# Kernel tuning notes

Measured on AMD Instinct MI355X. Metric: run time of the kernel, lower is better.

## Reference

```python
import jax, jax.numpy as jnp
import numpy as np
import math

B, N, DIM = 16, 1024, 384
DEPTH, HEADS, DH = 6, 6, 64
INNER = HEADS * DH          # 384
MLP = 1536
LN_EPS = 1e-5


def setup_inputs() -> dict:
    key = jax.random.key(0)
    ks = jax.random.split(key, 7)
    s = 0.02
    x = jax.random.normal(ks[0], (B, N, DIM), dtype=jnp.float32)
    ln1_g = jnp.ones((DEPTH, DIM), jnp.float32)
    ln1_b = jnp.zeros((DEPTH, DIM), jnp.float32)
    qkv_w = jax.random.normal(ks[1], (DEPTH, DIM, 3 * INNER), jnp.float32) * s
    temp = jnp.full((DEPTH,), math.log(DH ** -0.5), jnp.float32)
    out_w = jax.random.normal(ks[2], (DEPTH, INNER, DIM), jnp.float32) * s
    out_b = jnp.zeros((DEPTH, DIM), jnp.float32)
    ln2_g = jnp.ones((DEPTH, DIM), jnp.float32)
    ln2_b = jnp.zeros((DEPTH, DIM), jnp.float32)
    ff_w1 = jax.random.normal(ks[3], (DEPTH, DIM, MLP), jnp.float32) * s
    ff_b1 = jnp.zeros((DEPTH, MLP), jnp.float32)
    ff_w2 = jax.random.normal(ks[4], (DEPTH, MLP, DIM), jnp.float32) * s
    ff_b2 = jnp.zeros((DEPTH, DIM), jnp.float32)
    return dict(x=x, ln1_g=ln1_g, ln1_b=ln1_b, qkv_w=qkv_w, temp=temp,
                out_w=out_w, out_b=out_b, ln2_g=ln2_g, ln2_b=ln2_b,
                ff_w1=ff_w1, ff_b1=ff_b1, ff_w2=ff_w2, ff_b2=ff_b2)


def _ln(x, g, b):
    m = jnp.mean(x, axis=-1, keepdims=True)
    v = jnp.var(x, axis=-1, keepdims=True)
    return (x - m) * jax.lax.rsqrt(v + LN_EPS) * g + b


def reference(x, ln1_g, ln1_b, qkv_w, temp, out_w, out_b,
              ln2_g, ln2_b, ff_w1, ff_b1, ff_w2, ff_b2):
    neg = -jnp.finfo(x.dtype).max
    eye = jnp.eye(N, dtype=bool)

    def step(x, p):
        g1, b1, wqkv, t, wo, bo, g2, b2, w1, bb1, w2, bb2 = p
        # --- PreNorm + LSA attention ---
        h = _ln(x, g1, b1)
        qkv = h @ wqkv                              # [B, N, 3*INNER]
        q, k, v = jnp.split(qkv, 3, axis=-1)
        split_heads = lambda a: a.reshape(B, N, HEADS, DH).transpose(0, 2, 1, 3)
        q, k, v = split_heads(q), split_heads(k), split_heads(v)
        dots = jnp.einsum('bhnd,bhmd->bhnm', q, k) * jnp.exp(t)
        dots = jnp.where(eye, neg, dots)            # mask diagonal (LSA)
        attn = jax.nn.softmax(dots, axis=-1)
        o = jnp.einsum('bhnm,bhmd->bhnd', attn, v)
        o = o.transpose(0, 2, 1, 3).reshape(B, N, INNER)
        x = x + o @ wo + bo
        # --- PreNorm + FeedForward (exact GELU) ---
        h2 = _ln(x, g2, b2)
        ff = jax.nn.gelu(h2 @ w1 + bb1, approximate=False) @ w2 + bb2
        x = x + ff
        return x, None

    params = (ln1_g, ln1_b, qkv_w, temp, out_w, out_b,
              ln2_g, ln2_b, ff_w1, ff_b1, ff_w2, ff_b2)
    x, _ = jax.lax.scan(step, x, params)
    return x
```

## Files before the change

### kernel.cpp

```cpp
#include <hip/hip_runtime.h>
#include <hip/hip_bf16.h>
#include <math.h>

#define B_     16
#define NTOK   1024
#define DIM_   384
#define DEPTH_ 6
#define HEADS_ 6
#define DH_    64
#define MLP_   1536
#define MTOT   (B_ * NTOK)
#define NBH    (B_ * HEADS_)
#define QKV_PLANE ((size_t)NBH * NTOK * DH_)

typedef unsigned short u16;
typedef unsigned int u32;
typedef short short8 __attribute__((ext_vector_type(8)));
typedef float f32x4 __attribute__((ext_vector_type(4)));

static __device__ __forceinline__ u16 f2b(float f) {
    __hip_bfloat16 h = __float2bfloat16(f);
    return *reinterpret_cast<u16*>(&h);
}

#define GLOAD_LDS16(gp, lp)                                                     \
    __builtin_amdgcn_global_load_lds(                                           \
        (const __attribute__((address_space(1))) void*)(gp),                    \
        (__attribute__((address_space(3))) void*)(lp), 16, 0, 0)

#define WAIT_VM(N)                                                              \
    do { asm volatile("s_waitcnt vmcnt(" #N ")" ::: "memory");                  \
         __builtin_amdgcn_sched_barrier(0); } while (0)
#define WAIT_LGKM0()                                                            \
    do { asm volatile("s_waitcnt lgkmcnt(0)" ::: "memory");                     \
         __builtin_amdgcn_sched_barrier(0); } while (0)

__launch_bounds__(256)
__global__ void transpose_w_kernel(const float* __restrict__ W, u16* __restrict__ WT,
                                   int K, int N) {
    const int layer = blockIdx.z;
    W  += (size_t)layer * K * N;
    WT += (size_t)layer * K * N;
    __shared__ u16 tile[64 * 72];
    const int t = threadIdx.x;
    const int k0 = blockIdx.x * 64, n0 = blockIdx.y * 64;
    const int row = t >> 2, cs = (t & 3) * 16;
    const float4* src = reinterpret_cast<const float4*>(W + (size_t)(k0 + row) * N + n0 + cs);
#pragma unroll
    for (int i = 0; i < 4; i++) {
        float4 f = src[i];
        tile[row * 72 + cs + i * 4 + 0] = f2b(f.x);
        tile[row * 72 + cs + i * 4 + 1] = f2b(f.y);
        tile[row * 72 + cs + i * 4 + 2] = f2b(f.z);
        tile[row * 72 + cs + i * 4 + 3] = f2b(f.w);
    }
    __syncthreads();
    const int nrow = row, ks = cs;
    u16 vals[16] __attribute__((aligned(16)));
#pragma unroll
    for (int e = 0; e < 16; e++) vals[e] = tile[(ks + e) * 72 + nrow];
    u16* dst = WT + (size_t)(n0 + nrow) * K + k0 + ks;
    *reinterpret_cast<short8*>(dst)     = *reinterpret_cast<short8*>(&vals[0]);
    *reinterpret_cast<short8*>(dst + 8) = *reinterpret_cast<short8*>(&vals[8]);
}

__launch_bounds__(256)
__global__ void ln_kernel(const float* __restrict__ x, const float* __restrict__ g,
                          const float* __restrict__ b, u16* __restrict__ h) {
    const int tok  = blockIdx.x * 4 + (threadIdx.x >> 6);
    const int lane = threadIdx.x & 63;
    const float* xr = x + (size_t)tok * DIM_;
    float v[6];
    float s = 0.f;
#pragma unroll
    for (int i = 0; i < 6; i++) { v[i] = xr[lane + i * 64]; s += v[i]; }
#pragma unroll
    for (int m = 1; m < 64; m <<= 1) s += __shfl_xor(s, m);
    const float mean = s * (1.f / 384.f);
    float qs = 0.f;
#pragma unroll
    for (int i = 0; i < 6; i++) { float d = v[i] - mean; qs += d * d; }
#pragma unroll
    for (int m = 1; m < 64; m <<= 1) qs += __shfl_xor(qs, m);
    const float inv = rsqrtf(qs * (1.f / 384.f) + 1e-5f);
    u16* hr = h + (size_t)tok * DIM_;
#pragma unroll
    for (int i = 0; i < 6; i++) {
        const int c = lane + i * 64;
        hr[c] = f2b((v[i] - mean) * inv * g[c] + b[c]);
    }
}

enum { EPI_QKV = 0, EPI_RES = 1, EPI_GELU = 2 };

template <int EPI>
__launch_bounds__(256)
__global__ void gemm_kernel(const u16* __restrict__ A, const u16* __restrict__ BT, int K,
                            int ntn,
                            const float* __restrict__ bias, const float* __restrict__ resid,
                            float* __restrict__ outf, u16* __restrict__ outb, int ldc,
                            u16* __restrict__ qkv_base) {
    __shared__ u16 As[3][4096];
    __shared__ u16 Bs[3][4096];
    const int t = threadIdx.x;
    const int lane = t & 63, w = t >> 6;
    const int wm = w >> 1, wn = w & 1;

    const int cpx = (int)gridDim.x >> 3;
    const int swz = ((int)blockIdx.x & 7) * cpx + ((int)blockIdx.x >> 3);
    const int m0 = (swz / ntn) * 128, n0 = (swz % ntn) * 128;

    f32x4 acc[4][4] = {};

    const int c0p = w * 1024, c1p = w * 1024 + 512;
    const int seg = (lane & 3) * 8;
    const u16* agp0 = A  + (size_t)(m0 + (w * 2 + 0) * 16 + (lane >> 2)) * K + seg;
    const u16* agp1 = A  + (size_t)(m0 + (w * 2 + 1) * 16 + (lane >> 2)) * K + seg;
    const u16* bgp0 = BT + (size_t)(n0 + (w * 2 + 0) * 16 + (lane >> 2)) * K + seg;
    const u16* bgp1 = BT + (size_t)(n0 + (w * 2 + 1) * 16 + (lane >> 2)) * K + seg;

    const int T = K >> 5;
    GLOAD_LDS16(agp0,      &As[0][c0p]);
    GLOAD_LDS16(agp1,      &As[0][c1p]);
    GLOAD_LDS16(bgp0,      &Bs[0][c0p]);
    GLOAD_LDS16(bgp1,      &Bs[0][c1p]);
    GLOAD_LDS16(agp0 + 32, &As[1][c0p]);
    GLOAD_LDS16(agp1 + 32, &As[1][c1p]);
    GLOAD_LDS16(bgp0 + 32, &Bs[1][c0p]);
    GLOAD_LDS16(bgp1 + 32, &Bs[1][c1p]);

    int b0 = 0, b1 = 1, b2 = 2;
    for (int tt = 0; tt < T; ++tt) {
        if (tt + 2 < T) {
            const int kk = (tt + 2) << 5;
            GLOAD_LDS16(agp0 + kk, &As[b2][c0p]);
            GLOAD_LDS16(agp1 + kk, &As[b2][c1p]);
            GLOAD_LDS16(bgp0 + kk, &Bs[b2][c0p]);
            GLOAD_LDS16(bgp1 + kk, &Bs[b2][c1p]);
            WAIT_VM(8);
        } else if (tt + 1 < T) {
            WAIT_VM(4);
        } else {
            WAIT_VM(0);
        }
        __builtin_amdgcn_s_barrier();
        short8 af[4], bf[4];
#pragma unroll
        for (int i = 0; i < 4; i++)
            af[i] = *reinterpret_cast<const short8*>(
                &As[b0][(wm * 64 + i * 16 + (lane & 15)) * 32 + (lane >> 4) * 8]);
#pragma unroll
        for (int j = 0; j < 4; j++)
            bf[j] = *reinterpret_cast<const short8*>(
                &Bs[b0][(wn * 64 + j * 16 + (lane & 15)) * 32 + (lane >> 4) * 8]);
#pragma unroll
        for (int i = 0; i < 4; i++)
#pragma unroll
            for (int j = 0; j < 4; j++)
                acc[i][j] = __builtin_amdgcn_mfma_f32_16x16x32_bf16(af[i], bf[j], acc[i][j], 0, 0, 0);
        WAIT_LGKM0();
        __builtin_amdgcn_s_barrier();
        const int tmp = b0; b0 = b1; b1 = b2; b2 = tmp;
    }

    const int rbase = (lane >> 4) * 4;
    const int cb = lane & 15;
#pragma unroll
    for (int i = 0; i < 4; i++) {
#pragma unroll
        for (int j = 0; j < 4; j++) {
            if constexpr (EPI == EPI_QKV) {
                const int c = n0 + wn * 64 + j * 16 + cb;
                const int which = c / 384;
                const int cc = c - which * 384;
                const int head = cc >> 6, dh = cc & 63;
                const int nb = m0 + wm * 64 + i * 16 + rbase;
                const int b = nb >> 10, nt = nb & 1023;
                const size_t bh = (size_t)(b * HEADS_ + head);
                if (which == 2) {
                    u16 pk[4] __attribute__((aligned(8)));
#pragma unroll
                    for (int r = 0; r < 4; r++) pk[r] = f2b(acc[i][j][r]);
                    const int nsw = (nt & ~63) | ((((nt >> 3) & 7) ^ (dh & 7)) << 3) | (nt & 7);
                    *reinterpret_cast<uint2*>(
                        &qkv_base[2 * QKV_PLANE + bh * 65536 + (size_t)dh * 1024 + nsw]) =
                        *reinterpret_cast<uint2*>(pk);
                } else if (which == 1) {
#pragma unroll
                    for (int r = 0; r < 4; r++) {
                        const int n = nt + r;
                        const int dsw = (((dh >> 3) ^ (n & 7)) << 3) | (dh & 7);
                        qkv_base[QKV_PLANE + bh * 65536 + (size_t)n * 64 + dsw] =
                            f2b(acc[i][j][r]);
                    }
                } else {
#pragma unroll
                    for (int r = 0; r < 4; r++)
                        qkv_base[bh * 65536 + (size_t)(nt + r) * 64 + dh] = f2b(acc[i][j][r]);
                }
            } else {
#pragma unroll
                for (int r = 0; r < 4; r++) {
                    const int m = m0 + wm * 64 + i * 16 + rbase + r;
                    const int c = n0 + wn * 64 + j * 16 + cb;
                    const float val = acc[i][j][r];
                    if constexpr (EPI == EPI_RES) {
                        outf[(size_t)m * ldc + c] = resid[(size_t)m * ldc + c] + bias[c] + val;
                    } else {
                        const float xg = val + bias[c];
                        const float y = 0.7978845608f * (xg + 0.044715f * xg * xg * xg);
                        const float e = __expf(2.0f * fabsf(y));
                        float th = 1.0f - 2.0f / (e + 1.0f);
                        th = copysignf(th, y);
                        outb[(size_t)m * ldc + c] = f2b(0.5f * xg * (1.0f + th));
                    }
                }
            }
        }
    }
}

__launch_bounds__(256)
__global__ void attn_kernel(const u16* __restrict__ q, const u16* __restrict__ k,
                            const u16* __restrict__ v, const float* __restrict__ temp,
                            u16* __restrict__ o) {
    __shared__ u16 Kt[2][4096];
    __shared__ u16 Vt[2][4096];
    __shared__ u16 Ps[4][16 * 80];
    const int t = threadIdx.x, lane = t & 63, w = t >> 6;
    const int g8 = lane >> 4, qi = lane & 15;
    const int bh = blockIdx.x, q0 = blockIdx.y * 64;
    const float scale2 = __expf(temp[0]) * 1.4426950408889634f;
    const size_t base = (size_t)bh * (NTOK * DH_);

    short8 bq[2];
#pragma unroll
    for (int s = 0; s < 2; s++)
        bq[s] = *reinterpret_cast<const short8*>(
            &q[base + (size_t)(q0 + w * 16 + qi) * 64 + s * 32 + g8 * 8]);

    float m_s = -3.0e38f, l_s = 0.f;
    f32x4 accO[4] = {};
    const int qglob = q0 + w * 16 + qi;

    const int srow = w * 8 + (lane >> 3);
    const int schunk = (lane & 7) * 8;
    const u16* kg0 = k + base + (size_t)srow * 64 + schunk;
    const u16* vg0 = v + base + (size_t)srow * 1024 + schunk;
    const int wp = w * 512;

    GLOAD_LDS16(kg0,             &Kt[0][wp]);
    GLOAD_LDS16(kg0 + 32 * 64,   &Kt[0][wp + 2048]);
    GLOAD_LDS16(vg0,             &Vt[0][wp]);
    GLOAD_LDS16(vg0 + 32 * 1024, &Vt[0][wp + 2048]);

    int cur = 0;
    for (int jt = 0; jt < 16; ++jt) {
        if (jt + 1 < 16) {
            const size_t jn = (size_t)(jt + 1) * 64;
            GLOAD_LDS16(kg0 + jn * 64,            &Kt[cur ^ 1][wp]);
            GLOAD_LDS16(kg0 + jn * 64 + 32 * 64,  &Kt[cur ^ 1][wp + 2048]);
            GLOAD_LDS16(vg0 + jn,                 &Vt[cur ^ 1][wp]);
            GLOAD_LDS16(vg0 + jn + 32 * 1024,     &Vt[cur ^ 1][wp + 2048]);
            WAIT_VM(4);
        } else {
            WAIT_VM(0);
        }
        __builtin_amdgcn_s_barrier();

        f32x4 sf[4] = {};
#pragma unroll
        for (int c = 0; c < 4; c++) {
            const int krow = c * 16 + qi;
#pragma unroll
            for (int s = 0; s < 2; s++) {
                short8 af = *reinterpret_cast<const short8*>(
                    &Kt[cur][krow * 64 + (((s * 4 + g8) ^ (krow & 7)) << 3)]);
                sf[c] = __builtin_amdgcn_mfma_f32_16x16x32_bf16(af, bq[s], sf[c], 0, 0, 0);
            }
        }

        float p[4][4];
        float vmax = -3.0e38f;
        if (jt * 64 == q0) {
#pragma unroll
            for (int c = 0; c < 4; c++)
#pragma unroll
                for (int r = 0; r < 4; r++) {
                    float sv = sf[c][r] * scale2;
                    if (jt * 64 + c * 16 + g8 * 4 + r == qglob) sv = -3.0e37f;
                    p[c][r] = sv;
                    vmax = fmaxf(vmax, sv);
                }
        } else {
#pragma unroll
            for (int c = 0; c < 4; c++)
#pragma unroll
                for (int r = 0; r < 4; r++) {
                    const float sv = sf[c][r] * scale2;
                    p[c][r] = sv;
                    vmax = fmaxf(vmax, sv);
                }
        }
        vmax = fmaxf(vmax, __shfl_xor(vmax, 16));
        vmax = fmaxf(vmax, __shfl_xor(vmax, 32));

        if (!__all(vmax - m_s <= 11.0f)) {
            const float mnew = fmaxf(m_s, vmax);
            const float alpha = exp2f(m_s - mnew);
            m_s = mnew;
            l_s *= alpha;
#pragma unroll
            for (int r = 0; r < 4; r++) {
                const float a_r = __shfl(alpha, g8 * 4 + r, 64);
#pragma unroll
                for (int g = 0; g < 4; g++) accO[g][r] *= a_r;
            }
        }

        float tsum = 0.f;
#pragma unroll
        for (int c = 0; c < 4; c++)
#pragma unroll
            for (int r = 0; r < 4; r++) {
                const float pe = exp2f(p[c][r] - m_s);
                p[c][r] = pe;
                tsum += pe;
            }
        tsum += __shfl_xor(tsum, 16);
        tsum += __shfl_xor(tsum, 32);
        l_s += tsum;

#pragma unroll
        for (int c = 0; c < 4; c++) {
            u32 lo = (u32)f2b(p[c][0]) | ((u32)f2b(p[c][1]) << 16);
            u32 hi = (u32)f2b(p[c][2]) | ((u32)f2b(p[c][3]) << 16);
            uint2 pr; pr.x = lo; pr.y = hi;
            *reinterpret_cast<uint2*>(&Ps[w][qi * 80 + c * 16 + g8 * 4]) = pr;
        }

#pragma unroll
        for (int s = 0; s < 2; s++) {
            short8 ap = *reinterpret_cast<const short8*>(&Ps[w][qi * 80 + s * 32 + g8 * 8]);
#pragma unroll
            for (int g = 0; g < 4; g++) {
                const int vrow = g * 16 + qi;
                short8 bv = *reinterpret_cast<const short8*>(
                    &Vt[cur][vrow * 64 + (((s * 4 + g8) ^ (vrow & 7)) << 3)]);
                accO[g] = __builtin_amdgcn_mfma_f32_16x16x32_bf16(ap, bv, accO[g], 0, 0, 0);
            }
        }
        WAIT_LGKM0();
        __builtin_amdgcn_s_barrier();
        cur ^= 1;
    }

    const int bidx = bh / HEADS_, head = bh % HEADS_;
#pragma unroll
    for (int r = 0; r < 4; r++) {
        const float li = __shfl(l_s, g8 * 4 + r, 64);
        const float linv = 1.f / li;
        const int n = q0 + w * 16 + g8 * 4 + r;
#pragma unroll
        for (int g = 0; g < 4; g++) {
            const int dh = g * 16 + qi;
            o[((size_t)(bidx * NTOK + n)) * DIM_ + head * DH_ + dh] = f2b(accO[g][r] * linv);
        }
    }
}

extern "C" void kernel_launch(void* const* d_in, const int* in_sizes, int n_in,
                              void* d_out, int out_size, void* d_ws, size_t ws_size,
                              hipStream_t stream) {
    const float* x_in  = (const float*)d_in[0];
    const float* ln1_g = (const float*)d_in[1];
    const float* ln1_b = (const float*)d_in[2];
    const float* qkv_w = (const float*)d_in[3];
    const float* temp  = (const float*)d_in[4];
    const float* out_w = (const float*)d_in[5];
    const float* out_b = (const float*)d_in[6];
    const float* ln2_g = (const float*)d_in[7];
    const float* ln2_b = (const float*)d_in[8];
    const float* ff_w1 = (const float*)d_in[9];
    const float* ff_b1 = (const float*)d_in[10];
    const float* ff_w2 = (const float*)d_in[11];
    const float* ff_b2 = (const float*)d_in[12];

    char* ws = (char*)d_ws;
    size_t off = 0;
    auto alloc = [&](size_t bytes) -> void* {
        void* p = ws + off;
        off += (bytes + 255) & ~(size_t)255;
        return p;
    };
    u16* wt_qkv = (u16*)alloc((size_t)DEPTH_ * 1152 * 384 * 2);
    u16* wt_out = (u16*)alloc((size_t)DEPTH_ * 384 * 384 * 2);
    u16* wt_ff1 = (u16*)alloc((size_t)DEPTH_ * 1536 * 384 * 2);
    u16* wt_ff2 = (u16*)alloc((size_t)DEPTH_ * 384 * 1536 * 2);
    u16* H      = (u16*)alloc((size_t)MTOT * DIM_ * 2);
    u16* QKV    = (u16*)alloc((size_t)MTOT * MLP_ * 2);
    u16* MID    = QKV;

    float* X = (float*)d_out;

    hipMemcpyAsync(X, x_in, (size_t)MTOT * DIM_ * sizeof(float),
                   hipMemcpyDeviceToDevice, stream);

    transpose_w_kernel<<<dim3(6, 18, DEPTH_), 256, 0, stream>>>(qkv_w, wt_qkv, 384, 1152);
    transpose_w_kernel<<<dim3(6, 6, DEPTH_), 256, 0, stream>>>(out_w, wt_out, 384, 384);
    transpose_w_kernel<<<dim3(6, 24, DEPTH_), 256, 0, stream>>>(ff_w1, wt_ff1, 384, 1536);
    transpose_w_kernel<<<dim3(24, 6, DEPTH_), 256, 0, stream>>>(ff_w2, wt_ff2, 1536, 384);

    for (int layer = 0; layer < DEPTH_; layer++) {
        ln_kernel<<<4096, 256, 0, stream>>>(X, ln1_g + layer * DIM_, ln1_b + layer * DIM_, H);
        gemm_kernel<EPI_QKV><<<dim3(128 * 9), 256, 0, stream>>>(
            H, wt_qkv + (size_t)layer * 1152 * 384, 384, 9,
            nullptr, nullptr, nullptr, nullptr, 0, QKV);
        attn_kernel<<<dim3(96, 16), 256, 0, stream>>>(
            QKV, QKV + QKV_PLANE, QKV + 2 * QKV_PLANE, temp + layer, H);
        gemm_kernel<EPI_RES><<<dim3(128 * 3), 256, 0, stream>>>(
            H, wt_out + (size_t)layer * 384 * 384, 384, 3,
            out_b + layer * DIM_, X, X, nullptr, DIM_, nullptr);
        ln_kernel<<<4096, 256, 0, stream>>>(X, ln2_g + layer * DIM_, ln2_b + layer * DIM_, H);
        gemm_kernel<EPI_GELU><<<dim3(128 * 12), 256, 0, stream>>>(
            H, wt_ff1 + (size_t)layer * 1536 * 384, 384, 12,
            ff_b1 + layer * MLP_, nullptr, nullptr, MID, MLP_, nullptr);
        gemm_kernel<EPI_RES><<<dim3(128 * 3), 256, 0, stream>>>(
            MID, wt_ff2 + (size_t)layer * 384 * 1536, 1536, 3,
            ff_b2 + layer * DIM_, X, X, nullptr, DIM_, nullptr);
    }
}
```

Before: 1.407 ms.

## Shrink GEMM tile to 128x64 with double buffering for more blocks and occupancy

The GEMM output tile is narrowed from 128x128 to 128x64, and LDS buffering drops from triple to double. Launch bounds now request 5 blocks per SM. Grid sizes double so the mostly small-N GEMMs (N=384) get more blocks and better CU coverage. The cost is less operand reuse per block, more A-tile reloads, and a shallower prefetch pipeline.

```diff
diff --git a/kernel.cpp b/kernel.cpp
--- a/kernel.cpp
+++ b/kernel.cpp
@@ -94,83 +94,75 @@
 enum { EPI_QKV = 0, EPI_RES = 1, EPI_GELU = 2 };
 
 template <int EPI>
-__launch_bounds__(256)
+__launch_bounds__(256, 5)
 __global__ void gemm_kernel(const u16* __restrict__ A, const u16* __restrict__ BT, int K,
                             int ntn,
                             const float* __restrict__ bias, const float* __restrict__ resid,
                             float* __restrict__ outf, u16* __restrict__ outb, int ldc,
                             u16* __restrict__ qkv_base) {
-    __shared__ u16 As[3][4096];
-    __shared__ u16 Bs[3][4096];
+    __shared__ u16 As[2][4096];
+    __shared__ u16 Bs[2][2048];
     const int t = threadIdx.x;
     const int lane = t & 63, w = t >> 6;
+    const int qi = lane & 15, g8 = lane >> 4;
     const int wm = w >> 1, wn = w & 1;
 
     const int cpx = (int)gridDim.x >> 3;
     const int swz = ((int)blockIdx.x & 7) * cpx + ((int)blockIdx.x >> 3);
-    const int m0 = (swz / ntn) * 128, n0 = (swz % ntn) * 128;
-
-    f32x4 acc[4][4] = {};
-
-    const int c0p = w * 1024, c1p = w * 1024 + 512;
+    const int m0 = (swz / ntn) * 128, n0 = (swz % ntn) * 64;
+
+    f32x4 acc[4][2] = {};
+
     const int seg = (lane & 3) * 8;
     const u16* agp0 = A  + (size_t)(m0 + (w * 2 + 0) * 16 + (lane >> 2)) * K + seg;
     const u16* agp1 = A  + (size_t)(m0 + (w * 2 + 1) * 16 + (lane >> 2)) * K + seg;
-    const u16* bgp0 = BT + (size_t)(n0 + (w * 2 + 0) * 16 + (lane >> 2)) * K + seg;
-    const u16* bgp1 = BT + (size_t)(n0 + (w * 2 + 1) * 16 + (lane >> 2)) * K + seg;
+    const u16* bgp  = BT + (size_t)(n0 + w * 16 + (lane >> 2)) * K + seg;
+    const int a0p = (w * 2) * 512, a1p = (w * 2 + 1) * 512, bp = w * 512;
 
     const int T = K >> 5;
-    GLOAD_LDS16(agp0,      &As[0][c0p]);
-    GLOAD_LDS16(agp1,      &As[0][c1p]);
-    GLOAD_LDS16(bgp0,      &Bs[0][c0p]);
-    GLOAD_LDS16(bgp1,      &Bs[0][c1p]);
-    GLOAD_LDS16(agp0 + 32, &As[1][c0p]);
-    GLOAD_LDS16(agp1 + 32, &As[1][c1p]);
-    GLOAD_LDS16(bgp0 + 32, &Bs[1][c0p]);
-    GLOAD_LDS16(bgp1 + 32, &Bs[1][c1p]);
-
-    int b0 = 0, b1 = 1, b2 = 2;
+    GLOAD_LDS16(agp0, &As[0][a0p]);
+    GLOAD_LDS16(agp1, &As[0][a1p]);
+    GLOAD_LDS16(bgp,  &Bs[0][bp]);
+
+    int cur = 0;
     for (int tt = 0; tt < T; ++tt) {
-        if (tt + 2 < T) {
-            const int kk = (tt + 2) << 5;
-            GLOAD_LDS16(agp0 + kk, &As[b2][c0p]);
-            GLOAD_LDS16(agp1 + kk, &As[b2][c1p]);
-            GLOAD_LDS16(bgp0 + kk, &Bs[b2][c0p]);
-            GLOAD_LDS16(bgp1 + kk, &Bs[b2][c1p]);
-            WAIT_VM(8);
-        } else if (tt + 1 < T) {
-            WAIT_VM(4);
+        if (tt + 1 < T) {
+            const int kk = (tt + 1) << 5;
+            GLOAD_LDS16(agp0 + kk, &As[cur ^ 1][a0p]);
+            GLOAD_LDS16(agp1 + kk, &As[cur ^ 1][a1p]);
+            GLOAD_LDS16(bgp + kk,  &Bs[cur ^ 1][bp]);
+            WAIT_VM(3);
         } else {
             WAIT_VM(0);
         }
         __builtin_amdgcn_s_barrier();
-        short8 af[4], bf[4];
+        short8 af[4], bf[2];
 #pragma unroll
         for (int i = 0; i < 4; i++)
             af[i] = *reinterpret_cast<const short8*>(
-                &As[b0][(wm * 64 + i * 16 + (lane & 15)) * 32 + (lane >> 4) * 8]);
-#pragma unroll
-        for (int j = 0; j < 4; j++)
+                &As[cur][(wm * 64 + i * 16 + qi) * 32 + g8 * 8]);
+#pragma unroll
+        for (int j = 0; j < 2; j++)
             bf[j] = *reinterpret_cast<const short8*>(
-                &Bs[b0][(wn * 64 + j * 16 + (lane & 15)) * 32 + (lane >> 4) * 8]);
+                &Bs[cur][(wn * 32 + j * 16 + qi) * 32 + g8 * 8]);
 #pragma unroll
         for (int i = 0; i < 4; i++)
 #pragma unroll
-            for (int j = 0; j < 4; j++)
+            for (int j = 0; j < 2; j++)
                 acc[i][j] = __builtin_amdgcn_mfma_f32_16x16x32_bf16(af[i], bf[j], acc[i][j], 0, 0, 0);
         WAIT_LGKM0();
         __builtin_amdgcn_s_barrier();
-        const int tmp = b0; b0 = b1; b1 = b2; b2 = tmp;
-    }
-
-    const int rbase = (lane >> 4) * 4;
-    const int cb = lane & 15;
+        cur ^= 1;
+    }
+
+    const int rbase = g8 * 4;
+    const int cb = qi;
 #pragma unroll
     for (int i = 0; i < 4; i++) {
 #pragma unroll
-        for (int j = 0; j < 4; j++) {
+        for (int j = 0; j < 2; j++) {
             if constexpr (EPI == EPI_QKV) {
-                const int c = n0 + wn * 64 + j * 16 + cb;
+                const int c = n0 + wn * 32 + j * 16 + cb;
                 const int which = c / 384;
                 const int cc = c - which * 384;
                 const int head = cc >> 6, dh = cc & 63;
@@ -202,7 +194,7 @@
 #pragma unroll
                 for (int r = 0; r < 4; r++) {
                     const int m = m0 + wm * 64 + i * 16 + rbase + r;
-                    const int c = n0 + wn * 64 + j * 16 + cb;
+                    const int c = n0 + wn * 32 + j * 16 + cb;
                     const float val = acc[i][j][r];
                     if constexpr (EPI == EPI_RES) {
                         outf[(size_t)m * ldc + c] = resid[(size_t)m * ldc + c] + bias[c] + val;
@@ -413,20 +405,20 @@
 
     for (int layer = 0; layer < DEPTH_; layer++) {
         ln_kernel<<<4096, 256, 0, stream>>>(X, ln1_g + layer * DIM_, ln1_b + layer * DIM_, H);
-        gemm_kernel<EPI_QKV><<<dim3(128 * 9), 256, 0, stream>>>(
-            H, wt_qkv + (size_t)layer * 1152 * 384, 384, 9,
+        gemm_kernel<EPI_QKV><<<dim3(128 * 18), 256, 0, stream>>>(
+            H, wt_qkv + (size_t)layer * 1152 * 384, 384, 18,
             nullptr, nullptr, nullptr, nullptr, 0, QKV);
         attn_kernel<<<dim3(96, 16), 256, 0, stream>>>(
             QKV, QKV + QKV_PLANE, QKV + 2 * QKV_PLANE, temp + layer, H);
-        gemm_kernel<EPI_RES><<<dim3(128 * 3), 256, 0, stream>>>(
-            H, wt_out + (size_t)layer * 384 * 384, 384, 3,
+        gemm_kernel<EPI_RES><<<dim3(128 * 6), 256, 0, stream>>>(
+            H, wt_out + (size_t)layer * 384 * 384, 384, 6,
             out_b + layer * DIM_, X, X, nullptr, DIM_, nullptr);
         ln_kernel<<<4096, 256, 0, stream>>>(X, ln2_g + layer * DIM_, ln2_b + layer * DIM_, H);
-        gemm_kernel<EPI_GELU><<<dim3(128 * 12), 256, 0, stream>>>(
-            H, wt_ff1 + (size_t)layer * 1536 * 384, 384, 12,
+        gemm_kernel<EPI_GELU><<<dim3(128 * 24), 256, 0, stream>>>(
+            H, wt_ff1 + (size_t)layer * 1536 * 384, 384, 24,
             ff_b1 + layer * MLP_, nullptr, nullptr, MID, MLP_, nullptr);
-        gemm_kernel<EPI_RES><<<dim3(128 * 3), 256, 0, stream>>>(
-            MID, wt_ff2 + (size_t)layer * 384 * 1536, 1536, 3,
+        gemm_kernel<EPI_RES><<<dim3(128 * 6), 256, 0, stream>>>(
+            MID, wt_ff2 + (size_t)layer * 384 * 1536, 1536, 6,
             ff_b2 + layer * DIM_, X, X, nullptr, DIM_, nullptr);
     }
 }
```

Result: slower. 1.443 ms (+2.6%).
